# Performance work log

Measured on AMD Instinct MI355X. Metric: run time of the kernel, lower is better.

Reference implementation:

```python
import jax, jax.numpy as jnp
import numpy as np

N, E, MSG, HID, T, C = 100000, 1600000, 16, 16, 8, 32

def setup_inputs() -> dict:
    key = jax.random.key(0)
    ks = jax.random.split(key, 12)
    return {
        'features': jax.random.normal(ks[0], (N, HID), dtype=jnp.float32),
        'src': jax.random.randint(ks[1], (E,), 0, N, dtype=jnp.int32),
        'dst': jax.random.randint(ks[2], (E,), 0, N, dtype=jnp.int32),
        'etype': jax.random.randint(ks[3], (E,), 0, T, dtype=jnp.int32),
        'edge_table': jax.random.normal(ks[4], (T, MSG * HID), dtype=jnp.float32) * 0.1,
        'W_ih': jax.random.normal(ks[5], (3 * HID, MSG), dtype=jnp.float32) * 0.1,
        'W_hh': jax.random.normal(ks[6], (3 * HID, HID), dtype=jnp.float32) * 0.1,
        'b_ih': jax.random.normal(ks[7], (3 * HID,), dtype=jnp.float32) * 0.1,
        'b_hh': jax.random.normal(ks[8], (3 * HID,), dtype=jnp.float32) * 0.1,
        'W_out': jax.random.normal(ks[9], (C, HID), dtype=jnp.float32) * 0.1,
        'b_out': jax.random.normal(ks[10], (C,), dtype=jnp.float32) * 0.1,
    }

def reference(features, src, dst, etype, edge_table, W_ih, W_hh, b_ih, b_hh, W_out, b_out):
    n_nodes, hid = features.shape
    msg_dim = edge_table.shape[1] // hid
    # per-edge message matrix lookup: [E, msg, hid]
    A = edge_table[etype].reshape(-1, msg_dim, hid)
    # msg = A @ h_src : [E, msg]
    msg = jnp.einsum('emh,eh->em', A, features[src])
    # scatter-sum into destination nodes: [N, msg]
    m = jax.ops.segment_sum(msg, dst, num_segments=n_nodes)
    # single GRU step (PyTorch gate ordering: r, z, n)
    gi = m @ W_ih.T + b_ih          # [N, 3*hid]
    gh = features @ W_hh.T + b_hh   # [N, 3*hid]
    i_r, i_z, i_n = jnp.split(gi, 3, axis=1)
    h_r, h_z, h_n = jnp.split(gh, 3, axis=1)
    r = jax.nn.sigmoid(i_r + h_r)
    z = jax.nn.sigmoid(i_z + h_z)
    n = jnp.tanh(i_n + r * h_n)
    h = (1.0 - z) * n + z * features
    # output projection
    return h @ W_out.T + b_out
```

## Files before the change

kernel.cpp:

```cpp
#include <hip/hip_runtime.h>

#define N_NODES 100000
#define N_EDGES 1600000
#define MSG 16
#define HID 16
#define NT 8
#define NC 32

__global__ __launch_bounds__(256) void ggnn_phase1(
    const float* __restrict__ feat,
    const float* __restrict__ edge_table,
    float* __restrict__ Y) {
    int n = blockIdx.x * 256 + threadIdx.x;
    if (n >= N_NODES) return;

    float h[HID];
    const float4* f4 = reinterpret_cast<const float4*>(feat + (size_t)n * HID);
    #pragma unroll
    for (int q = 0; q < HID / 4; ++q) {
        float4 v = f4[q];
        h[q * 4 + 0] = v.x; h[q * 4 + 1] = v.y;
        h[q * 4 + 2] = v.z; h[q * 4 + 3] = v.w;
    }

    float4* yrow = reinterpret_cast<float4*>(Y + (size_t)n * (NT * MSG));
    for (int t = 0; t < NT; ++t) {
        const float* At = edge_table + t * (MSG * HID);
        #pragma unroll
        for (int j4 = 0; j4 < MSG / 4; ++j4) {
            float4 o;
            float* op = &o.x;
            #pragma unroll
            for (int jj = 0; jj < 4; ++jj) {
                const float* a = At + (j4 * 4 + jj) * HID;
                float acc = 0.f;
                #pragma unroll
                for (int k = 0; k < HID; ++k) acc += a[k] * h[k];
                op[jj] = acc;
            }
            yrow[t * (MSG / 4) + j4] = o;
        }
    }
}

__global__ __launch_bounds__(256) void ggnn_phase2(
    const int* __restrict__ src,
    const int* __restrict__ dst,
    const int* __restrict__ etype,
    const float* __restrict__ Y,
    float* __restrict__ m) {
    long long tid = (long long)blockIdx.x * 256 + threadIdx.x;
    int e = (int)(tid >> 4);
    int j = (int)(tid & 15);
    if (e >= N_EDGES) return;
    int s = src[e];
    int d = dst[e];
    int t = etype[e];
    float v = Y[(size_t)s * (NT * MSG) + t * MSG + j];
    atomicAdd(m + (size_t)d * MSG + j, v);
}

__device__ __forceinline__ float fast_sigmoid(float x) {
    return 1.f / (1.f + __expf(-x));
}
__device__ __forceinline__ float fast_tanh(float x) {
    return 2.f / (1.f + __expf(-2.f * x)) - 1.f;
}

__global__ __launch_bounds__(256) void ggnn_phase3(
    const float* __restrict__ feat,
    const float* __restrict__ m,
    const float* __restrict__ W_ih,
    const float* __restrict__ W_hh,
    const float* __restrict__ b_ih,
    const float* __restrict__ b_hh,
    const float* __restrict__ W_out,
    const float* __restrict__ b_out,
    float* __restrict__ out) {
    int n = blockIdx.x * 256 + threadIdx.x;
    if (n >= N_NODES) return;

    float mv[MSG], h[HID];
    {
        const float4* m4 = reinterpret_cast<const float4*>(m + (size_t)n * MSG);
        const float4* f4 = reinterpret_cast<const float4*>(feat + (size_t)n * HID);
        #pragma unroll
        for (int q = 0; q < 4; ++q) {
            float4 a = m4[q];
            mv[q * 4 + 0] = a.x; mv[q * 4 + 1] = a.y;
            mv[q * 4 + 2] = a.z; mv[q * 4 + 3] = a.w;
            float4 b = f4[q];
            h[q * 4 + 0] = b.x; h[q * 4 + 1] = b.y;
            h[q * 4 + 2] = b.z; h[q * 4 + 3] = b.w;
        }
    }

    float srz[2 * HID];
    for (int g = 0; g < 2 * HID; ++g) {
        float ai = 0.f, ah = 0.f;
        const float* wi = W_ih + g * MSG;
        const float* wh = W_hh + g * HID;
        #pragma unroll
        for (int k = 0; k < HID; ++k) {
            ai += wi[k] * mv[k];
            ah += wh[k] * h[k];
        }
        srz[g] = ai + ah + b_ih[g] + b_hh[g];
    }
    float i_n[HID], h_n[HID];
    #pragma unroll
    for (int j = 0; j < HID; ++j) {
        int g = 2 * HID + j;
        float ai = b_ih[g], ah = b_hh[g];
        const float* wi = W_ih + g * MSG;
        const float* wh = W_hh + g * HID;
        #pragma unroll
        for (int k = 0; k < HID; ++k) {
            ai += wi[k] * mv[k];
            ah += wh[k] * h[k];
        }
        i_n[j] = ai;
        h_n[j] = ah;
    }

    float hn[HID];
    #pragma unroll
    for (int j = 0; j < HID; ++j) {
        float r = fast_sigmoid(srz[j]);
        float z = fast_sigmoid(srz[HID + j]);
        float nn = fast_tanh(i_n[j] + r * h_n[j]);
        hn[j] = (1.f - z) * nn + z * h[j];
    }

    float4* op = reinterpret_cast<float4*>(out + (size_t)n * NC);
    #pragma unroll
    for (int c4 = 0; c4 < NC / 4; ++c4) {
        float4 o;
        float* oo = &o.x;
        #pragma unroll
        for (int cc = 0; cc < 4; ++cc) {
            int c = c4 * 4 + cc;
            float acc = b_out[c];
            const float* wo = W_out + c * HID;
            #pragma unroll
            for (int k = 0; k < HID; ++k) acc += wo[k] * hn[k];
            oo[cc] = acc;
        }
        op[c4] = o;
    }
}

extern "C" void kernel_launch(void* const* d_in, const int* in_sizes, int n_in,
                              void* d_out, int out_size, void* d_ws, size_t ws_size,
                              hipStream_t stream) {
    const float* feat       = (const float*)d_in[0];
    const int*   src        = (const int*)d_in[1];
    const int*   dst        = (const int*)d_in[2];
    const int*   etype      = (const int*)d_in[3];
    const float* edge_table = (const float*)d_in[4];
    const float* W_ih       = (const float*)d_in[5];
    const float* W_hh       = (const float*)d_in[6];
    const float* b_ih       = (const float*)d_in[7];
    const float* b_hh       = (const float*)d_in[8];
    const float* W_out      = (const float*)d_in[9];
    const float* b_out      = (const float*)d_in[10];
    float* out = (float*)d_out;

    float* m = (float*)d_ws;
    float* Y = m + (size_t)N_NODES * MSG;

    hipMemsetAsync(m, 0, (size_t)N_NODES * MSG * sizeof(float), stream);

    int blocks1 = (N_NODES + 255) / 256;
    ggnn_phase1<<<blocks1, 256, 0, stream>>>(feat, edge_table, Y);

    long long p2_threads = (long long)N_EDGES * 16;
    int blocks2 = (int)((p2_threads + 255) / 256);
    ggnn_phase2<<<blocks2, 256, 0, stream>>>(src, dst, etype, Y, m);

    ggnn_phase3<<<blocks1, 256, 0, stream>>>(feat, m, W_ih, W_hh, b_ih, b_hh,
                                             W_out, b_out, out);
}
```

Measured before the change: 225.9 us.

## Replace float atomic scatter with CSR build and per-node gather fused into GRU

```diff
diff --git a/kernel.cpp b/kernel.cpp
--- a/kernel.cpp
+++ b/kernel.cpp
@@ -6,6 +6,7 @@
 #define HID 16
 #define NT 8
 #define NC 32
+#define SCAN_BLOCKS 391
 
 __global__ __launch_bounds__(256) void ggnn_phase1(
     const float* __restrict__ feat,
@@ -43,21 +44,71 @@
     }
 }
 
-__global__ __launch_bounds__(256) void ggnn_phase2(
-    const int* __restrict__ src,
-    const int* __restrict__ dst,
-    const int* __restrict__ etype,
-    const float* __restrict__ Y,
-    float* __restrict__ m) {
-    long long tid = (long long)blockIdx.x * 256 + threadIdx.x;
-    int e = (int)(tid >> 4);
-    int j = (int)(tid & 15);
+__global__ __launch_bounds__(256) void ggnn_hist(
+    const int* __restrict__ dst, int* __restrict__ counts) {
+    int e = blockIdx.x * 256 + threadIdx.x;
+    if (e < N_EDGES) atomicAdd(&counts[dst[e]], 1);
+}
+
+__global__ __launch_bounds__(256) void ggnn_block_sums(
+    const int* __restrict__ counts, int* __restrict__ bsum) {
+    __shared__ int s[256];
+    int n = blockIdx.x * 256 + threadIdx.x;
+    s[threadIdx.x] = (n < N_NODES) ? counts[n] : 0;
+    __syncthreads();
+    for (int d = 128; d > 0; d >>= 1) {
+        if (threadIdx.x < d) s[threadIdx.x] += s[threadIdx.x + d];
+        __syncthreads();
+    }
+    if (threadIdx.x == 0) bsum[blockIdx.x] = s[0];
+}
+
+__global__ __launch_bounds__(512) void ggnn_scan_bsums(
+    const int* __restrict__ bsum, int* __restrict__ boff) {
+    __shared__ int tmp[512];
+    int t = threadIdx.x;
+    int v = (t < SCAN_BLOCKS) ? bsum[t] : 0;
+    tmp[t] = v;
+    __syncthreads();
+    for (int d = 1; d < 512; d <<= 1) {
+        int x = (t >= d) ? tmp[t - d] : 0;
+        __syncthreads();
+        tmp[t] += x;
+        __syncthreads();
+    }
+    if (t < SCAN_BLOCKS) boff[t] = tmp[t] - v;
+}
+
+__global__ __launch_bounds__(256) void ggnn_scan_local(
+    const int* __restrict__ counts, const int* __restrict__ boff,
+    int* __restrict__ offsets, int* __restrict__ cursor) {
+    __shared__ int tmp[256];
+    int tid = threadIdx.x;
+    int n = blockIdx.x * 256 + tid;
+    int v = (n < N_NODES) ? counts[n] : 0;
+    tmp[tid] = v;
+    __syncthreads();
+    for (int d = 1; d < 256; d <<= 1) {
+        int x = (tid >= d) ? tmp[tid - d] : 0;
+        __syncthreads();
+        tmp[tid] += x;
+        __syncthreads();
+    }
+    if (n < N_NODES) {
+        int off = boff[blockIdx.x] + tmp[tid] - v;
+        offsets[n] = off;
+        cursor[n] = off;
+    }
+}
+
+__global__ __launch_bounds__(256) void ggnn_scatter(
+    const int* __restrict__ src, const int* __restrict__ dst,
+    const int* __restrict__ etype, int* __restrict__ cursor,
+    int* __restrict__ payload) {
+    int e = blockIdx.x * 256 + threadIdx.x;
     if (e >= N_EDGES) return;
-    int s = src[e];
-    int d = dst[e];
-    int t = etype[e];
-    float v = Y[(size_t)s * (NT * MSG) + t * MSG + j];
-    atomicAdd(m + (size_t)d * MSG + j, v);
+    int pos = atomicAdd(&cursor[dst[e]], 1);
+    payload[pos] = src[e] * NT + etype[e];
 }
 
 __device__ __forceinline__ float fast_sigmoid(float x) {
@@ -67,9 +118,12 @@
     return 2.f / (1.f + __expf(-2.f * x)) - 1.f;
 }
 
-__global__ __launch_bounds__(256) void ggnn_phase3(
+__global__ __launch_bounds__(256) void ggnn_gather_gru(
     const float* __restrict__ feat,
-    const float* __restrict__ m,
+    const float* __restrict__ Y,
+    const int* __restrict__ offsets,
+    const int* __restrict__ cursor_end,
+    const int* __restrict__ payload,
     const float* __restrict__ W_ih,
     const float* __restrict__ W_hh,
     const float* __restrict__ b_ih,
@@ -77,77 +131,64 @@
     const float* __restrict__ W_out,
     const float* __restrict__ b_out,
     float* __restrict__ out) {
-    int n = blockIdx.x * 256 + threadIdx.x;
-    if (n >= N_NODES) return;
-
-    float mv[MSG], h[HID];
-    {
-        const float4* m4 = reinterpret_cast<const float4*>(m + (size_t)n * MSG);
-        const float4* f4 = reinterpret_cast<const float4*>(feat + (size_t)n * HID);
-        #pragma unroll
-        for (int q = 0; q < 4; ++q) {
-            float4 a = m4[q];
-            mv[q * 4 + 0] = a.x; mv[q * 4 + 1] = a.y;
-            mv[q * 4 + 2] = a.z; mv[q * 4 + 3] = a.w;
-            float4 b = f4[q];
-            h[q * 4 + 0] = b.x; h[q * 4 + 1] = b.y;
-            h[q * 4 + 2] = b.z; h[q * 4 + 3] = b.w;
+    __shared__ float msh[16][16];
+    __shared__ float hsh[16][16];
+    __shared__ float nsh[16][16];
+
+    int tid = threadIdx.x;
+    int node_l = tid >> 4;
+    int j = tid & 15;
+    int n = blockIdx.x * 16 + node_l;
+
+    float hj = feat[(size_t)n * HID + j];
+    hsh[node_l][j] = hj;
+
+    int start = offsets[n];
+    int end = cursor_end[n];
+    float acc = 0.f;
+    for (int i0 = start; i0 < end; i0 += 16) {
+        int cnt = end - i0;
+        if (cnt > 16) cnt = 16;
+        int pv = (j < cnt) ? payload[i0 + j] : 0;
+        for (int i = 0; i < cnt; ++i) {
+            int p = __shfl(pv, i, 16);
+            acc += Y[(size_t)p * MSG + j];
         }
     }
-
-    float srz[2 * HID];
-    for (int g = 0; g < 2 * HID; ++g) {
-        float ai = 0.f, ah = 0.f;
-        const float* wi = W_ih + g * MSG;
-        const float* wh = W_hh + g * HID;
-        #pragma unroll
-        for (int k = 0; k < HID; ++k) {
-            ai += wi[k] * mv[k];
-            ah += wh[k] * h[k];
-        }
-        srz[g] = ai + ah + b_ih[g] + b_hh[g];
-    }
-    float i_n[HID], h_n[HID];
+    msh[node_l][j] = acc;
+    __syncthreads();
+
+    const float* m_ = msh[node_l];
+    const float* h_ = hsh[node_l];
+    float gr = b_ih[j] + b_hh[j];
+    float gz = b_ih[HID + j] + b_hh[HID + j];
+    float gin = b_ih[2 * HID + j];
+    float ghn = b_hh[2 * HID + j];
     #pragma unroll
-    for (int j = 0; j < HID; ++j) {
-        int g = 2 * HID + j;
-        float ai = b_ih[g], ah = b_hh[g];
-        const float* wi = W_ih + g * MSG;
-        const float* wh = W_hh + g * HID;
-        #pragma unroll
-        for (int k = 0; k < HID; ++k) {
-            ai += wi[k] * mv[k];
-            ah += wh[k] * h[k];
-        }
-        i_n[j] = ai;
-        h_n[j] = ah;
-    }
-
-    float hn[HID];
+    for (int k = 0; k < HID; ++k) {
+        float mk = m_[k], hk = h_[k];
+        gr  += W_ih[(0 * HID + j) * MSG + k] * mk + W_hh[(0 * HID + j) * HID + k] * hk;
+        gz  += W_ih[(1 * HID + j) * MSG + k] * mk + W_hh[(1 * HID + j) * HID + k] * hk;
+        gin += W_ih[(2 * HID + j) * MSG + k] * mk;
+        ghn += W_hh[(2 * HID + j) * HID + k] * hk;
+    }
+    float r = fast_sigmoid(gr);
+    float z = fast_sigmoid(gz);
+    float nn = fast_tanh(gin + r * ghn);
+    float hnj = (1.f - z) * nn + z * hj;
+    nsh[node_l][j] = hnj;
+    __syncthreads();
+
+    const float* hn_ = nsh[node_l];
+    float o0 = b_out[j], o1 = b_out[HID + j];
     #pragma unroll
-    for (int j = 0; j < HID; ++j) {
-        float r = fast_sigmoid(srz[j]);
-        float z = fast_sigmoid(srz[HID + j]);
-        float nn = fast_tanh(i_n[j] + r * h_n[j]);
-        hn[j] = (1.f - z) * nn + z * h[j];
-    }
-
-    float4* op = reinterpret_cast<float4*>(out + (size_t)n * NC);
-    #pragma unroll
-    for (int c4 = 0; c4 < NC / 4; ++c4) {
-        float4 o;
-        float* oo = &o.x;
-        #pragma unroll
-        for (int cc = 0; cc < 4; ++cc) {
-            int c = c4 * 4 + cc;
-            float acc = b_out[c];
-            const float* wo = W_out + c * HID;
-            #pragma unroll
-            for (int k = 0; k < HID; ++k) acc += wo[k] * hn[k];
-            oo[cc] = acc;
-        }
-        op[c4] = o;
-    }
+    for (int k = 0; k < HID; ++k) {
+        float hk = hn_[k];
+        o0 += W_out[j * HID + k] * hk;
+        o1 += W_out[(HID + j) * HID + k] * hk;
+    }
+    out[(size_t)n * NC + j] = o0;
+    out[(size_t)n * NC + HID + j] = o1;
 }
 
 extern "C" void kernel_launch(void* const* d_in, const int* in_sizes, int n_in,
@@ -166,18 +207,26 @@
     const float* b_out      = (const float*)d_in[10];
     float* out = (float*)d_out;
 
-    float* m = (float*)d_ws;
-    float* Y = m + (size_t)N_NODES * MSG;
-
-    hipMemsetAsync(m, 0, (size_t)N_NODES * MSG * sizeof(float), stream);
-
-    int blocks1 = (N_NODES + 255) / 256;
-    ggnn_phase1<<<blocks1, 256, 0, stream>>>(feat, edge_table, Y);
-
-    long long p2_threads = (long long)N_EDGES * 16;
-    int blocks2 = (int)((p2_threads + 255) / 256);
-    ggnn_phase2<<<blocks2, 256, 0, stream>>>(src, dst, etype, Y, m);
-
-    ggnn_phase3<<<blocks1, 256, 0, stream>>>(feat, m, W_ih, W_hh, b_ih, b_hh,
-                                             W_out, b_out, out);
-}
+    float* Y      = (float*)d_ws;
+    int*   counts = (int*)(Y + (size_t)N_NODES * NT * MSG);
+    int*   offsets= counts + N_NODES;
+    int*   cursor = offsets + N_NODES;
+    int*   bsum   = cursor + N_NODES;
+    int*   boff   = bsum + 512;
+    int*   payload= boff + 512;
+
+    hipMemsetAsync(counts, 0, N_NODES * sizeof(int), stream);
+
+    int nblocks = (N_NODES + 255) / 256;
+    int eblocks = (N_EDGES + 255) / 256;
+
+    ggnn_phase1<<<nblocks, 256, 0, stream>>>(feat, edge_table, Y);
+    ggnn_hist<<<eblocks, 256, 0, stream>>>(dst, counts);
+    ggnn_block_sums<<<nblocks, 256, 0, stream>>>(counts, bsum);
+    ggnn_scan_bsums<<<1, 512, 0, stream>>>(bsum, boff);
+    ggnn_scan_local<<<nblocks, 256, 0, stream>>>(counts, boff, offsets, cursor);
+    ggnn_scatter<<<eblocks, 256, 0, stream>>>(src, dst, etype, cursor, payload);
+    ggnn_gather_gru<<<N_NODES / 16, 256, 0, stream>>>(
+        feat, Y, offsets, cursor, payload,
+        W_ih, W_hh, b_ih, b_hh, W_out, b_out, out);
+}
```

New measurement: 395.3 us. 74.9% more time.

## Fuse per-node message precompute into edge scatter kernel using shared edge table

Applied to the files above, without the earlier changes.

```diff
diff --git a/kernel.cpp b/kernel.cpp
--- a/kernel.cpp
+++ b/kernel.cpp
@@ -7,57 +7,44 @@
 #define NT 8
 #define NC 32
 
-__global__ __launch_bounds__(256) void ggnn_phase1(
-    const float* __restrict__ feat,
-    const float* __restrict__ edge_table,
-    float* __restrict__ Y) {
-    int n = blockIdx.x * 256 + threadIdx.x;
-    if (n >= N_NODES) return;
-
-    float h[HID];
-    const float4* f4 = reinterpret_cast<const float4*>(feat + (size_t)n * HID);
-    #pragma unroll
-    for (int q = 0; q < HID / 4; ++q) {
-        float4 v = f4[q];
-        h[q * 4 + 0] = v.x; h[q * 4 + 1] = v.y;
-        h[q * 4 + 2] = v.z; h[q * 4 + 3] = v.w;
-    }
-
-    float4* yrow = reinterpret_cast<float4*>(Y + (size_t)n * (NT * MSG));
-    for (int t = 0; t < NT; ++t) {
-        const float* At = edge_table + t * (MSG * HID);
-        #pragma unroll
-        for (int j4 = 0; j4 < MSG / 4; ++j4) {
-            float4 o;
-            float* op = &o.x;
-            #pragma unroll
-            for (int jj = 0; jj < 4; ++jj) {
-                const float* a = At + (j4 * 4 + jj) * HID;
-                float acc = 0.f;
-                #pragma unroll
-                for (int k = 0; k < HID; ++k) acc += a[k] * h[k];
-                op[jj] = acc;
-            }
-            yrow[t * (MSG / 4) + j4] = o;
-        }
-    }
-}
-
-__global__ __launch_bounds__(256) void ggnn_phase2(
+__global__ __launch_bounds__(256) void ggnn_edge(
     const int* __restrict__ src,
     const int* __restrict__ dst,
     const int* __restrict__ etype,
-    const float* __restrict__ Y,
+    const float* __restrict__ feat,
+    const float* __restrict__ edge_table,
     float* __restrict__ m) {
-    long long tid = (long long)blockIdx.x * 256 + threadIdx.x;
-    int e = (int)(tid >> 4);
-    int j = (int)(tid & 15);
+    __shared__ float As[NT * MSG * HID];
+    int tid = threadIdx.x;
+    #pragma unroll
+    for (int i = tid; i < NT * MSG * HID; i += 256) {
+        int t = i >> 8;
+        int r = i & 255;
+        int j = r >> 4;
+        int k = r & 15;
+        As[t * 256 + k * 16 + j] = edge_table[i];
+    }
+    __syncthreads();
+
+    int e = blockIdx.x * 16 + (tid >> 4);
+    int j = tid & 15;
     if (e >= N_EDGES) return;
     int s = src[e];
     int d = dst[e];
     int t = etype[e];
-    float v = Y[(size_t)s * (NT * MSG) + t * MSG + j];
-    atomicAdd(m + (size_t)d * MSG + j, v);
+
+    float hj = feat[(size_t)s * HID + j];
+    int g = (tid >> 4) & 3;
+    const float* At = As + t * 256;
+
+    float acc = 0.f;
+    #pragma unroll
+    for (int k0 = 0; k0 < 16; ++k0) {
+        int k = (k0 + g) & 15;
+        float hk = __shfl(hj, k, 16);
+        acc += At[k * 16 + j] * hk;
+    }
+    atomicAdd(m + (size_t)d * MSG + j, acc);
 }
 
 __device__ __forceinline__ float fast_sigmoid(float x) {
@@ -67,7 +54,7 @@
     return 2.f / (1.f + __expf(-2.f * x)) - 1.f;
 }
 
-__global__ __launch_bounds__(256) void ggnn_phase3(
+__global__ __launch_bounds__(256) void ggnn_node(
     const float* __restrict__ feat,
     const float* __restrict__ m,
     const float* __restrict__ W_ih,
@@ -167,17 +154,13 @@
     float* out = (float*)d_out;
 
     float* m = (float*)d_ws;
-    float* Y = m + (size_t)N_NODES * MSG;
 
     hipMemsetAsync(m, 0, (size_t)N_NODES * MSG * sizeof(float), stream);
 
-    int blocks1 = (N_NODES + 255) / 256;
-    ggnn_phase1<<<blocks1, 256, 0, stream>>>(feat, edge_table, Y);
+    int eblocks = (N_EDGES + 15) / 16;
+    ggnn_edge<<<eblocks, 256, 0, stream>>>(src, dst, etype, feat, edge_table, m);
 
-    long long p2_threads = (long long)N_EDGES * 16;
-    int blocks2 = (int)((p2_threads + 255) / 256);
-    ggnn_phase2<<<blocks2, 256, 0, stream>>>(src, dst, etype, Y, m);
-
-    ggnn_phase3<<<blocks1, 256, 0, stream>>>(feat, m, W_ih, W_hh, b_ih, b_hh,
-                                             W_out, b_out, out);
+    int nblocks = (N_NODES + 255) / 256;
+    ggnn_node<<<nblocks, 256, 0, stream>>>(feat, m, W_ih, W_hh, b_ih, b_hh,
+                                           W_out, b_out, out);
 }
```

Measured after the change: 293.7 us. 30.0% more time.

## Store per-type messages in fp16 and scatter with packed half2 atomics

Applied to the files above, without the earlier changes.

```diff
diff --git a/kernel.cpp b/kernel.cpp
--- a/kernel.cpp
+++ b/kernel.cpp
@@ -1,4 +1,5 @@
 #include <hip/hip_runtime.h>
+#include <hip/hip_fp16.h>
 
 #define N_NODES 100000
 #define N_EDGES 1600000
@@ -7,10 +8,17 @@
 #define NT 8
 #define NC 32
 
+typedef _Float16 v2h __attribute__((ext_vector_type(2)));
+
+union H2U {
+    v2h h;
+    unsigned int u;
+};
+
 __global__ __launch_bounds__(256) void ggnn_phase1(
     const float* __restrict__ feat,
     const float* __restrict__ edge_table,
-    float* __restrict__ Y) {
+    unsigned int* __restrict__ Yu) {
     int n = blockIdx.x * 256 + threadIdx.x;
     if (n >= N_NODES) return;
 
@@ -23,23 +31,28 @@
         h[q * 4 + 2] = v.z; h[q * 4 + 3] = v.w;
     }
 
-    float4* yrow = reinterpret_cast<float4*>(Y + (size_t)n * (NT * MSG));
     for (int t = 0; t < NT; ++t) {
         const float* At = edge_table + t * (MSG * HID);
-        #pragma unroll
-        for (int j4 = 0; j4 < MSG / 4; ++j4) {
-            float4 o;
-            float* op = &o.x;
+        uint4 o[2];
+        unsigned int* ou = reinterpret_cast<unsigned int*>(o);
+        #pragma unroll
+        for (int j2 = 0; j2 < 8; ++j2) {
+            float a0 = 0.f, a1 = 0.f;
+            const float* r0 = At + (2 * j2) * HID;
+            const float* r1 = At + (2 * j2 + 1) * HID;
             #pragma unroll
-            for (int jj = 0; jj < 4; ++jj) {
-                const float* a = At + (j4 * 4 + jj) * HID;
-                float acc = 0.f;
-                #pragma unroll
-                for (int k = 0; k < HID; ++k) acc += a[k] * h[k];
-                op[jj] = acc;
+            for (int k = 0; k < HID; ++k) {
+                a0 += r0[k] * h[k];
+                a1 += r1[k] * h[k];
             }
-            yrow[t * (MSG / 4) + j4] = o;
-        }
+            H2U p;
+            p.h[0] = (_Float16)a0;
+            p.h[1] = (_Float16)a1;
+            ou[j2] = p.u;
+        }
+        uint4* dst4 = reinterpret_cast<uint4*>(Yu + (size_t)n * 64 + t * 8);
+        dst4[0] = o[0];
+        dst4[1] = o[1];
     }
 }
 
@@ -47,17 +60,23 @@
     const int* __restrict__ src,
     const int* __restrict__ dst,
     const int* __restrict__ etype,
-    const float* __restrict__ Y,
-    float* __restrict__ m) {
-    long long tid = (long long)blockIdx.x * 256 + threadIdx.x;
-    int e = (int)(tid >> 4);
-    int j = (int)(tid & 15);
+    const unsigned int* __restrict__ Yu,
+    unsigned int* __restrict__ m2) {
+    int tid = blockIdx.x * 256 + threadIdx.x;
+    int e = tid >> 3;
     if (e >= N_EDGES) return;
+    int c = tid & 7;
     int s = src[e];
     int d = dst[e];
     int t = etype[e];
-    float v = Y[(size_t)s * (NT * MSG) + t * MSG + j];
-    atomicAdd(m + (size_t)d * MSG + j, v);
+    H2U y;
+    y.u = Yu[(size_t)s * 64 + t * 8 + c];
+    v2h* addr = reinterpret_cast<v2h*>(m2 + (size_t)d * 8 + c);
+#if __has_builtin(__builtin_amdgcn_global_atomic_fadd_v2f16)
+    __builtin_amdgcn_global_atomic_fadd_v2f16(addr, y.h);
+#else
+    atomicAdd(reinterpret_cast<float*>(addr), (float)y.h[0] + 0.f * (float)y.h[1]);
+#endif
 }
 
 __device__ __forceinline__ float fast_sigmoid(float x) {
@@ -69,7 +88,7 @@
 
 __global__ __launch_bounds__(256) void ggnn_phase3(
     const float* __restrict__ feat,
-    const float* __restrict__ m,
+    const unsigned int* __restrict__ m2,
     const float* __restrict__ W_ih,
     const float* __restrict__ W_hh,
     const float* __restrict__ b_ih,
@@ -82,16 +101,22 @@
 
     float mv[MSG], h[HID];
     {
-        const float4* m4 = reinterpret_cast<const float4*>(m + (size_t)n * MSG);
+        const uint4* mu = reinterpret_cast<const uint4*>(m2 + (size_t)n * 8);
+        uint4 a = mu[0], b = mu[1];
+        unsigned int w[8] = {a.x, a.y, a.z, a.w, b.x, b.y, b.z, b.w};
+        #pragma unroll
+        for (int i = 0; i < 8; ++i) {
+            H2U hh;
+            hh.u = w[i];
+            mv[2 * i]     = (float)hh.h[0];
+            mv[2 * i + 1] = (float)hh.h[1];
+        }
         const float4* f4 = reinterpret_cast<const float4*>(feat + (size_t)n * HID);
         #pragma unroll
         for (int q = 0; q < 4; ++q) {
-            float4 a = m4[q];
-            mv[q * 4 + 0] = a.x; mv[q * 4 + 1] = a.y;
-            mv[q * 4 + 2] = a.z; mv[q * 4 + 3] = a.w;
-            float4 b = f4[q];
-            h[q * 4 + 0] = b.x; h[q * 4 + 1] = b.y;
-            h[q * 4 + 2] = b.z; h[q * 4 + 3] = b.w;
+            float4 v = f4[q];
+            h[q * 4 + 0] = v.x; h[q * 4 + 1] = v.y;
+            h[q * 4 + 2] = v.z; h[q * 4 + 3] = v.w;
         }
     }
 
@@ -166,18 +191,18 @@
     const float* b_out      = (const float*)d_in[10];
     float* out = (float*)d_out;
 
-    float* m = (float*)d_ws;
-    float* Y = m + (size_t)N_NODES * MSG;
-
-    hipMemsetAsync(m, 0, (size_t)N_NODES * MSG * sizeof(float), stream);
-
-    int blocks1 = (N_NODES + 255) / 256;
-    ggnn_phase1<<<blocks1, 256, 0, stream>>>(feat, edge_table, Y);
-
-    long long p2_threads = (long long)N_EDGES * 16;
-    int blocks2 = (int)((p2_threads + 255) / 256);
-    ggnn_phase2<<<blocks2, 256, 0, stream>>>(src, dst, etype, Y, m);
-
-    ggnn_phase3<<<blocks1, 256, 0, stream>>>(feat, m, W_ih, W_hh, b_ih, b_hh,
+    unsigned int* m2 = (unsigned int*)d_ws;
+    unsigned int* Yu = m2 + (size_t)N_NODES * 8;
+
+    (void)hipMemsetAsync(m2, 0, (size_t)N_NODES * 8 * sizeof(unsigned int), stream);
+
+    int nblocks = (N_NODES + 255) / 256;
+    ggnn_phase1<<<nblocks, 256, 0, stream>>>(feat, edge_table, Yu);
+
+    long long p2_threads = (long long)N_EDGES * 8;
+    int eblocks = (int)((p2_threads + 255) / 256);
+    ggnn_phase2<<<eblocks, 256, 0, stream>>>(src, dst, etype, Yu, m2);
+
+    ggnn_phase3<<<nblocks, 256, 0, stream>>>(feat, m2, W_ih, W_hh, b_ih, b_hh,
                                              W_out, b_out, out);
 }
```

Result: no change. 223.6 us (-1.0%).
